# Performance work log

Hardware: AMD Instinct MI355X
Metric: run time of the kernel (lower is better)

Reference implementation:

```python
import jax, jax.numpy as jnp
import numpy as np

B, T, P, D, L = 16, 120, 96, 128, 2


def setup_inputs() -> dict:
    key = jax.random.key(0)
    k1, k2, k3, k4 = jax.random.split(key, 4)
    x = jax.random.normal(k1, (B, P, D, T), dtype=jnp.float32)
    # distances: symmetric-ish positive pairwise distances from random 3D points
    pts = jax.random.uniform(k2, (B, T, P, 3), dtype=jnp.float32) * 5.0
    diff = pts[:, :, :, None, :] - pts[:, :, None, :, :]
    distances = jnp.sqrt(jnp.sum(diff * diff, axis=-1) + 1e-12)
    # contiguous-prefix padding mask (matches the original self-loop loop semantics)
    counts = jax.random.randint(k3, (B,), P // 2, P + 1)
    padding_mask = jnp.arange(P)[None, :] < counts[:, None]
    # params: xavier_uniform with gain 1e-5 ~ tiny; bias 0; LN gamma=1, beta=0
    limit = 1e-5 * np.sqrt(6.0 / (D + D))
    W = jax.random.uniform(k4, (L, D, D), minval=-limit, maxval=limit, dtype=jnp.float32)
    b = jnp.zeros((L, D), dtype=jnp.float32)
    gamma = jnp.ones((L, D), dtype=jnp.float32)
    beta = jnp.zeros((L, D), dtype=jnp.float32)
    return {"x": x, "distances": distances, "padding_mask": padding_mask,
            "W": W, "b": b, "gamma": gamma, "beta": beta}


def _build_adjacency(distances, padding_mask):
    # valid_mask: [B,T,P,P]
    vm2d = (padding_mask[:, :, None] & padding_mask[:, None, :]).astype(distances.dtype)  # [B,P,P]
    vm = vm2d[:, None, :, :]
    vd = distances * vm
    pos = (vd > 0).astype(distances.dtype)
    n = jnp.sum(pos)
    mean = jnp.sum(vd * pos) / n
    var = jnp.sum(((vd - mean) ** 2) * pos) / (n - 1.0)  # unbiased, as torch.std
    sigma = jnp.sqrt(var) + 1e-8
    adj = jnp.exp(-(distances ** 2) / (2.0 * sigma ** 2)) * vm
    # self loops on valid (contiguous-prefix) nodes: add diag(mask)
    eye_mask = jnp.eye(P, dtype=distances.dtype)[None, :, :] * padding_mask[:, :, None].astype(distances.dtype)
    adj = adj + eye_mask[:, None, :, :]
    # symmetric normalization D^{-1/2} A D^{-1/2}
    deg = jnp.clip(jnp.sum(adj, axis=-1, keepdims=True), 1e-8, None)  # [B,T,P,1]
    deg = jnp.clip(deg * padding_mask[:, None, :, None].astype(distances.dtype), 1e-8, None)
    dis = deg ** -0.5
    adj = dis * adj * jnp.swapaxes(dis, -2, -1)
    return adj * vm


def _layer_norm_D(x, g, bt, eps=1e-5):
    # x: [B,P,D,T]; normalize over D axis
    mu = jnp.mean(x, axis=2, keepdims=True)
    var = jnp.mean((x - mu) ** 2, axis=2, keepdims=True)
    return (x - mu) * jax.lax.rsqrt(var + eps) * g[None, None, :, None] + bt[None, None, :, None]


def reference(x, distances, padding_mask, W, b, gamma, beta):
    adj = _build_adjacency(distances, padding_mask)  # [B,T,P,P]
    mask_f = padding_mask.astype(x.dtype)
    for l in range(L):
        xt = jnp.transpose(x, (0, 3, 1, 2))                      # [B,T,P,D]
        h = jnp.einsum('btpd,de->btpe', xt, W[l])                # x @ W
        o = jnp.einsum('btpq,btqd->btpd', adj, h)                # A @ xW
        o = jax.nn.relu(o + b[l])
        o = o * mask_f[:, None, :, None]
        o = jnp.transpose(o, (0, 2, 3, 1))                       # [B,P,D,T]
        o = _layer_norm_D(o, gamma[l], beta[l])
        x = x + o
    return x
```

## Files before the change

### kernel.cpp

```cpp
#include <hip/hip_runtime.h>
#include <math.h>

typedef __bf16 bf16_t;
typedef __bf16 bf16x8 __attribute__((ext_vector_type(8)));
typedef __bf16 bf16x4 __attribute__((ext_vector_type(4)));
typedef float f32x4 __attribute__((ext_vector_type(4)));

namespace {
constexpr int kB = 16;
constexpr int kT = 120;
constexpr int kP = 96;
constexpr int kD = 128;
constexpr int kBT = kB * kT;
constexpr int kPP = kP * kP;
constexpr int kPD = kP * kD;
constexpr long long kND = (long long)kBT * kPP;
constexpr unsigned kND4 = (unsigned)(kND / 4);

constexpr int TIN_TILES_PER_B = kPD / 32;
constexpr int TIN_BLOCKS = TIN_TILES_PER_B * kB;
constexpr int PREP_BLOCKS = 128;
constexpr int STATS_BLOCKS = 1024;
constexpr int FRONT_BLOCKS = TIN_BLOCKS + PREP_BLOCKS + STATS_BLOCKS;

constexpr int YS = 136;
constexpr int HS = 104;
constexpr int OS = 132;
constexpr int AS = 104;
constexpr int HT_OFF = 26112;
constexpr int AL_OFF = 52736;
constexpr int MROW_OFF = 72704;
constexpr int DIS_OFF = 73088;
constexpr int SMEM_B = 73472;
}

__device__ __forceinline__ f32x4 mfma16(bf16x8 a, bf16x8 b, f32x4 c) {
    return __builtin_amdgcn_mfma_f32_16x16x32_bf16(a, b, c, 0, 0, 0);
}

__global__ __launch_bounds__(256) void k_front(const float* __restrict__ x,
                                               bf16_t* __restrict__ y,
                                               const float* __restrict__ dist,
                                               const unsigned char* __restrict__ mraw,
                                               int* __restrict__ mask,
                                               double* __restrict__ stats,
                                               const float* __restrict__ W,
                                               bf16_t* __restrict__ wT) {
    __shared__ __align__(16) char sm[15488];
    const int bid = blockIdx.x;
    const int tid = threadIdx.x;

    if (bid < TIN_BLOCKS) {
        float* tile = (float*)sm;
        int b = bid / TIN_TILES_PER_B;
        int pd0 = (bid - b * TIN_TILES_PER_B) * 32;
        const float* xb = x + ((long long)b * kPD + pd0) * kT;
        #pragma unroll
        for (int k = 0; k < 4; ++k) {
            int idx = k * 256 + tid;
            if (idx < 960) {
                int r = idx / 30, c = idx - r * 30;
                float4 v = *(const float4*)(xb + idx * 4);
                tile[r * 121 + c * 4 + 0] = v.x;
                tile[r * 121 + c * 4 + 1] = v.y;
                tile[r * 121 + c * 4 + 2] = v.z;
                tile[r * 121 + c * 4 + 3] = v.w;
            }
        }
        __syncthreads();
        bf16_t* yb = y + (long long)b * kT * kPD + pd0;
        #pragma unroll
        for (int k = 0; k < 2; ++k) {
            int idx = k * 256 + tid;
            if (idx < 480) {
                int t = idx >> 2, dg = idx & 3;
                bf16x8 o;
                #pragma unroll
                for (int j = 0; j < 8; ++j) o[j] = (bf16_t)tile[(dg * 8 + j) * 121 + t];
                *(bf16x8*)(yb + (long long)t * kPD + dg * 8) = o;
            }
        }
    } else if (bid < TIN_BLOCKS + PREP_BLOCKS) {
        int pb = bid - TIN_BLOCKS;
        int l = pb >> 6;
        int idx = (pb & 63) * 256 + tid;
        int n = idx >> 7, k = idx & 127;
        wT[l * 16384 + n * 128 + k] = (bf16_t)W[l * 16384 + k * 128 + n];

        if (pb == 0) {
            const unsigned int* u32 = (const unsigned int*)mraw;
            unsigned int w0 = u32[0];
            int mode;
            if (w0 == 0x01010101u) mode = 0;
            else if (w0 == 1u) mode = 1;
            else mode = 2;
            for (int i = tid; i < kB * kP; i += 256) {
                int v;
                if (mode == 0)      v = (mraw[i] != 0);
                else if (mode == 1) v = (u32[i] != 0);
                else                v = (((const float*)mraw)[i] != 0.0f);
                mask[i] = v;
            }
        }
    } else {
        int sb = bid - TIN_BLOCKS - PREP_BLOCKS;
        int* ml = (int*)sm;
        double* sh = (double*)(sm + 6144);
        {
            const unsigned int* u32 = (const unsigned int*)mraw;
            unsigned int w0 = u32[0];
            int mode;
            if (w0 == 0x01010101u) mode = 0;
            else if (w0 == 1u) mode = 1;
            else mode = 2;
            for (int i = tid; i < kB * kP; i += 256) {
                int v;
                if (mode == 0)      v = (mraw[i] != 0);
                else if (mode == 1) v = (u32[i] != 0);
                else                v = (((const float*)mraw)[i] != 0.0f);
                ml[i] = v;
            }
        }
        __syncthreads();

        unsigned stride = (unsigned)STATS_BLOCKS * 256u;
        double s = 0.0, s2 = 0.0;
        int cnt = 0;
        for (unsigned i4 = (unsigned)sb * 256u + (unsigned)tid; i4 < kND4; i4 += stride) {
            unsigned q0 = (i4 % 24u) * 4u;
            unsigned r = i4 / 24u;
            unsigned p = r % 96u;
            unsigned b = r / (96u * 120u);
            const int* mb = ml + b * kP;
            if (mb[p]) {
                float4 d4 = *(const float4*)(dist + (size_t)i4 * 4);
                if (mb[q0 + 0]) { s += d4.x; s2 += (double)d4.x * d4.x; cnt++; }
                if (mb[q0 + 1]) { s += d4.y; s2 += (double)d4.y * d4.y; cnt++; }
                if (mb[q0 + 2]) { s += d4.z; s2 += (double)d4.z * d4.z; cnt++; }
                if (mb[q0 + 3]) { s += d4.w; s2 += (double)d4.w * d4.w; cnt++; }
            }
        }
        sh[tid] = s; __syncthreads();
        for (int off = 128; off > 0; off >>= 1) { if (tid < off) sh[tid] += sh[tid + off]; __syncthreads(); }
        if (tid == 0) atomicAdd(&stats[0], sh[0]);
        __syncthreads();
        sh[tid] = s2; __syncthreads();
        for (int off = 128; off > 0; off >>= 1) { if (tid < off) sh[tid] += sh[tid + off]; __syncthreads(); }
        if (tid == 0) atomicAdd(&stats[1], sh[0]);
        __syncthreads();
        sh[tid] = (double)cnt; __syncthreads();
        for (int off = 128; off > 0; off >>= 1) { if (tid < off) sh[tid] += sh[tid + off]; __syncthreads(); }
        if (tid == 0) atomicAdd(&stats[2], sh[0]);
    }
}

__global__ __launch_bounds__(256) void k_tout(const bf16_t* __restrict__ y,
                                              float* __restrict__ out) {
    __shared__ float tile[64 * 121];
    int b = blockIdx.y, pd0 = blockIdx.x * 64;
    int tid = threadIdx.x;
    const bf16_t* yb = y + (long long)b * kT * kPD + pd0;
    #pragma unroll
    for (int k = 0; k < 4; ++k) {
        int idx = k * 256 + tid;
        if (idx < 960) {
            int t = idx >> 3, dg = idx & 7;
            bf16x8 v = *(const bf16x8*)(yb + (long long)t * kPD + dg * 8);
            #pragma unroll
            for (int j = 0; j < 8; ++j) tile[(dg * 8 + j) * 121 + t] = (float)v[j];
        }
    }
    __syncthreads();
    float* ob = out + ((long long)b * kPD + pd0) * kT;
    #pragma unroll
    for (int k = 0; k < 8; ++k) {
        int idx = k * 256 + tid;
        if (idx < 1920) {
            int r = idx / 30, c = idx - r * 30;
            float4 v;
            v.x = tile[r * 121 + c * 4 + 0];
            v.y = tile[r * 121 + c * 4 + 1];
            v.z = tile[r * 121 + c * 4 + 2];
            v.w = tile[r * 121 + c * 4 + 3];
            *(float4*)(ob + r * kT + c * 4) = v;
        }
    }
}

__global__ __launch_bounds__(512, 2) void k_gcn(bf16_t* __restrict__ y,
                                                const float* __restrict__ dist,
                                                const int* __restrict__ mask,
                                                const double* __restrict__ stats,
                                                const bf16_t* __restrict__ wT,
                                                const float* __restrict__ bias,
                                                const float* __restrict__ gamma,
                                                const float* __restrict__ beta) {
    __shared__ __align__(16) char smem[SMEM_B];
    bf16_t* yL  = (bf16_t*)smem;
    bf16_t* hT  = (bf16_t*)(smem + HT_OFF);
    bf16_t* oLb = (bf16_t*)(smem + HT_OFF);
    float*  aT  = (float*)smem;
    bf16_t* aL  = (bf16_t*)(smem + AL_OFF);
    float* mrowf = (float*)(smem + MROW_OFF);
    float* dis   = (float*)(smem + DIS_OFF);

    const int tid = threadIdx.x;
    const int tx = tid & 15, ty = tid >> 4;
    const int lane = tid & 63, w = tid >> 6;
    const int wm = w >> 2, wn = w & 3;
    const int fc = lane & 15, fg = lane >> 4;
    const int bt = blockIdx.x, b = bt / kT;
    const int d0 = tx * 8;

    bf16_t* ybt = y + (size_t)bt * kPD;
    const float* dbt = dist + (size_t)bt * kPP;

    if (tid < kP) mrowf[tid] = (float)mask[b * kP + tid];

    double sn = stats[2];
    double mean = stats[0] / sn;
    double var = (stats[1] - sn * mean * mean) / (sn - 1.0);
    double sg = sqrt(var) + 1e-8;
    float inv2s2 = (float)(1.0 / (2.0 * sg * sg));

    __syncthreads();

    #pragma unroll
    for (int k = 0; k < 5; ++k) {
        int i4 = k * 512 + tid;
        if (i4 < 2304) {
            int e = i4 * 4;
            int p = e / kP, q = e - p * kP;
            float4 d4 = *(const float4*)(dbt + e);
            float mp = mrowf[p];
            float vv[4];
            vv[0] = (mp * mrowf[q + 0] != 0.f) ? __expf(-d4.x * d4.x * inv2s2) : 0.f;
            vv[1] = (mp * mrowf[q + 1] != 0.f) ? __expf(-d4.y * d4.y * inv2s2) : 0.f;
            vv[2] = (mp * mrowf[q + 2] != 0.f) ? __expf(-d4.z * d4.z * inv2s2) : 0.f;
            vv[3] = (mp * mrowf[q + 3] != 0.f) ? __expf(-d4.w * d4.w * inv2s2) : 0.f;
            #pragma unroll
            for (int j = 0; j < 4; ++j) {
                if (p == q + j) vv[j] += mp;
                aT[p * 100 + q + j] = vv[j];
            }
        }
    }
    __syncthreads();

    if (tid < kP) {
        float s = 0.f;
        for (int q = 0; q < kP; ++q) s += aT[q * 100 + tid];
        s = fmaxf(s, 1e-8f);
        s = fmaxf(s * mrowf[tid], 1e-8f);
        dis[tid] = rsqrtf(s);
    }
    __syncthreads();

    #pragma unroll
    for (int k = 0; k < 5; ++k) {
        int i4 = k * 512 + tid;
        if (i4 < 2304) {
            int e = i4 * 4;
            int p = e / kP, q = e - p * kP;
            float dp = dis[p];
            bf16x4 ov;
            #pragma unroll
            for (int j = 0; j < 4; ++j)
                ov[j] = (bf16_t)(dp * aT[p * 100 + q + j] * dis[q + j]);
            *(bf16x4*)(aL + p * AS + q) = ov;
        }
    }
    __syncthreads();

    #pragma unroll
    for (int i = 0; i < 3; ++i) {
        int p = ty * 3 + i;
        *(bf16x8*)(yL + p * YS + d0) = *(const bf16x8*)(ybt + p * kD + d0);
    }

    for (int l = 0; l < 2; ++l) {
        const bf16_t* wTl = wT + l * kD * kD;
        bf16x8 wf[4][2];
        #pragma unroll
        for (int kt = 0; kt < 4; ++kt) {
            wf[kt][0] = *(const bf16x8*)(wTl + ((wn * 2 + 0) * 16 + fc) * kD + kt * 32 + fg * 8);
            wf[kt][1] = *(const bf16x8*)(wTl + ((wn * 2 + 1) * 16 + fc) * kD + kt * 32 + fg * 8);
        }
        __syncthreads();

        f32x4 acc[3][2];
        #pragma unroll
        for (int mt = 0; mt < 3; ++mt) { acc[mt][0] = {0,0,0,0}; acc[mt][1] = {0,0,0,0}; }
        #pragma unroll
        for (int kt = 0; kt < 4; ++kt) {
            #pragma unroll
            for (int mt = 0; mt < 3; ++mt) {
                bf16x8 af = *(const bf16x8*)(yL + ((wm * 3 + mt) * 16 + fc) * YS + kt * 32 + fg * 8);
                acc[mt][0] = mfma16(af, wf[kt][0], acc[mt][0]);
                acc[mt][1] = mfma16(af, wf[kt][1], acc[mt][1]);
            }
        }
        #pragma unroll
        for (int mt = 0; mt < 3; ++mt)
            #pragma unroll
            for (int nn = 0; nn < 2; ++nn) {
                int e = (wn * 2 + nn) * 16 + fc;
                int p0 = (wm * 3 + mt) * 16 + fg * 4;
                bf16x4 hv = {(bf16_t)acc[mt][nn][0], (bf16_t)acc[mt][nn][1],
                             (bf16_t)acc[mt][nn][2], (bf16_t)acc[mt][nn][3]};
                *(bf16x4*)(hT + e * HS + p0) = hv;
            }
        __syncthreads();

        f32x4 acc2[3][2];
        #pragma unroll
        for (int mt = 0; mt < 3; ++mt) { acc2[mt][0] = {0,0,0,0}; acc2[mt][1] = {0,0,0,0}; }
        #pragma unroll
        for (int kt = 0; kt < 3; ++kt) {
            bf16x8 bf0 = *(const bf16x8*)(hT + ((wn * 2 + 0) * 16 + fc) * HS + kt * 32 + fg * 8);
            bf16x8 bf1 = *(const bf16x8*)(hT + ((wn * 2 + 1) * 16 + fc) * HS + kt * 32 + fg * 8);
            #pragma unroll
            for (int mt = 0; mt < 3; ++mt) {
                bf16x8 af = *(const bf16x8*)(aL + ((wm * 3 + mt) * 16 + fc) * AS + kt * 32 + fg * 8);
                acc2[mt][0] = mfma16(af, bf0, acc2[mt][0]);
                acc2[mt][1] = mfma16(af, bf1, acc2[mt][1]);
            }
        }
        __syncthreads();

        #pragma unroll
        for (int mt = 0; mt < 3; ++mt)
            #pragma unroll
            for (int nn = 0; nn < 2; ++nn) {
                int d = (wn * 2 + nn) * 16 + fc;
                int p0 = (wm * 3 + mt) * 16 + fg * 4;
                oLb[(p0 + 0) * OS + d] = (bf16_t)acc2[mt][nn][0];
                oLb[(p0 + 1) * OS + d] = (bf16_t)acc2[mt][nn][1];
                oLb[(p0 + 2) * OS + d] = (bf16_t)acc2[mt][nn][2];
                oLb[(p0 + 3) * OS + d] = (bf16_t)acc2[mt][nn][3];
            }
        __syncthreads();

        const float* bl = bias + l * kD;
        const float* gl = gamma + l * kD;
        const float* bel = beta + l * kD;
        float4 bb0 = *(const float4*)(bl + d0), bb1 = *(const float4*)(bl + d0 + 4);
        float4 gg0 = *(const float4*)(gl + d0), gg1 = *(const float4*)(gl + d0 + 4);
        float4 be0 = *(const float4*)(bel + d0), be1 = *(const float4*)(bel + d0 + 4);
        float bb[8] = {bb0.x, bb0.y, bb0.z, bb0.w, bb1.x, bb1.y, bb1.z, bb1.w};
        float gg[8] = {gg0.x, gg0.y, gg0.z, gg0.w, gg1.x, gg1.y, gg1.z, gg1.w};
        float be[8] = {be0.x, be0.y, be0.z, be0.w, be1.x, be1.y, be1.z, be1.w};

        #pragma unroll
        for (int i = 0; i < 3; ++i) {
            int p = ty * 3 + i;
            float mpf = mrowf[p];
            bf16x4 o0 = *(const bf16x4*)(oLb + p * OS + d0);
            bf16x4 o1 = *(const bf16x4*)(oLb + p * OS + d0 + 4);
            bf16x8 yv = *(const bf16x8*)(yL + p * YS + d0);
            float v[8];
            #pragma unroll
            for (int j = 0; j < 4; ++j) {
                v[j]     = fmaxf((float)o0[j] + bb[j], 0.f) * mpf;
                v[j + 4] = fmaxf((float)o1[j] + bb[j + 4], 0.f) * mpf;
            }
            float s = v[0] + v[1] + v[2] + v[3] + v[4] + v[5] + v[6] + v[7];
            s += __shfl_xor(s, 8);
            s += __shfl_xor(s, 4);
            s += __shfl_xor(s, 2);
            s += __shfl_xor(s, 1);
            float mu = s * 0.0078125f;

            float ss = 0.f;
            #pragma unroll
            for (int j = 0; j < 8; ++j) { float dv = v[j] - mu; ss += dv * dv; }
            ss += __shfl_xor(ss, 8);
            ss += __shfl_xor(ss, 4);
            ss += __shfl_xor(ss, 2);
            ss += __shfl_xor(ss, 1);
            float inv = rsqrtf(ss * 0.0078125f + 1e-5f);

            bf16x8 c;
            #pragma unroll
            for (int j = 0; j < 8; ++j)
                c[j] = (bf16_t)((float)yv[j] + (v[j] - mu) * inv * gg[j] + be[j]);

            if (l == 0) {
                *(bf16x8*)(yL + p * YS + d0) = c;
            } else {
                *(bf16x8*)(ybt + p * kD + d0) = c;
            }
        }
    }
}

extern "C" void kernel_launch(void* const* d_in, const int* in_sizes, int n_in,
                              void* d_out, int out_size, void* d_ws, size_t ws_size,
                              hipStream_t stream) {
    (void)in_sizes; (void)n_in; (void)out_size; (void)ws_size;

    const float* x = (const float*)d_in[0];
    const float* dist = (const float*)d_in[1];
    const unsigned char* mraw = (const unsigned char*)d_in[2];
    const float* W = (const float*)d_in[3];
    const float* bias = (const float*)d_in[4];
    const float* gamma = (const float*)d_in[5];
    const float* beta = (const float*)d_in[6];
    float* out = (float*)d_out;

    char* ws = (char*)d_ws;
    double* stats = (double*)ws;
    int* mask = (int*)(ws + 64);
    bf16_t* wT = (bf16_t*)(ws + 8192);
    bf16_t* y = (bf16_t*)(ws + 81920);

    hipMemsetAsync(stats, 0, 32, stream);

    k_front<<<FRONT_BLOCKS, 256, 0, stream>>>(x, y, dist, mraw, mask, stats, W, wT);

    k_gcn<<<kBT, 512, 0, stream>>>(y, dist, mask, stats, wT, bias, gamma, beta);

    k_tout<<<dim3(kPD / 64, kB), 256, 0, stream>>>(y, out);
}
```

Before: 177.0 us.

## Prefetch transpose tiles across multiple 64-row tiles per block and double stats blocks

The x-transpose part of the front kernel now handles 64-row tiles, three per block, and holds the next tile's global loads in registers while the current tile is written out. This is meant to overlap global loads with the LDS transpose and to cut block count and launch overhead. The prep blocks now come first in the grid order, and the stats section gets twice as many blocks, presumably for more parallelism in the reduction. The trade-offs are higher register and shared memory use per block (30976 bytes of LDS), which may lower occupancy, and a reliance on the stats code handling the new block count correctly.

```diff
diff --git a/kernel.cpp b/kernel.cpp
--- a/kernel.cpp
+++ b/kernel.cpp
@@ -17,11 +17,12 @@
 constexpr long long kND = (long long)kBT * kPP;
 constexpr unsigned kND4 = (unsigned)(kND / 4);
 
-constexpr int TIN_TILES_PER_B = kPD / 32;
-constexpr int TIN_BLOCKS = TIN_TILES_PER_B * kB;
 constexpr int PREP_BLOCKS = 128;
-constexpr int STATS_BLOCKS = 1024;
-constexpr int FRONT_BLOCKS = TIN_BLOCKS + PREP_BLOCKS + STATS_BLOCKS;
+constexpr int TIN_TILES = (kPD / 64) * kB;
+constexpr int TILES_PER_BLOCK = 3;
+constexpr int TIN_BLOCKS = TIN_TILES / TILES_PER_BLOCK;
+constexpr int STATS_BLOCKS = 2048;
+constexpr int FRONT_BLOCKS = PREP_BLOCKS + TIN_BLOCKS + STATS_BLOCKS;
 
 constexpr int YS = 136;
 constexpr int HS = 104;
@@ -46,42 +47,12 @@
                                                double* __restrict__ stats,
                                                const float* __restrict__ W,
                                                bf16_t* __restrict__ wT) {
-    __shared__ __align__(16) char sm[15488];
+    __shared__ __align__(16) char sm[30976];
     const int bid = blockIdx.x;
     const int tid = threadIdx.x;
 
-    if (bid < TIN_BLOCKS) {
-        float* tile = (float*)sm;
-        int b = bid / TIN_TILES_PER_B;
-        int pd0 = (bid - b * TIN_TILES_PER_B) * 32;
-        const float* xb = x + ((long long)b * kPD + pd0) * kT;
-        #pragma unroll
-        for (int k = 0; k < 4; ++k) {
-            int idx = k * 256 + tid;
-            if (idx < 960) {
-                int r = idx / 30, c = idx - r * 30;
-                float4 v = *(const float4*)(xb + idx * 4);
-                tile[r * 121 + c * 4 + 0] = v.x;
-                tile[r * 121 + c * 4 + 1] = v.y;
-                tile[r * 121 + c * 4 + 2] = v.z;
-                tile[r * 121 + c * 4 + 3] = v.w;
-            }
-        }
-        __syncthreads();
-        bf16_t* yb = y + (long long)b * kT * kPD + pd0;
-        #pragma unroll
-        for (int k = 0; k < 2; ++k) {
-            int idx = k * 256 + tid;
-            if (idx < 480) {
-                int t = idx >> 2, dg = idx & 3;
-                bf16x8 o;
-                #pragma unroll
-                for (int j = 0; j < 8; ++j) o[j] = (bf16_t)tile[(dg * 8 + j) * 121 + t];
-                *(bf16x8*)(yb + (long long)t * kPD + dg * 8) = o;
-            }
-        }
-    } else if (bid < TIN_BLOCKS + PREP_BLOCKS) {
-        int pb = bid - TIN_BLOCKS;
+    if (bid < PREP_BLOCKS) {
+        int pb = bid;
         int l = pb >> 6;
         int idx = (pb & 63) * 256 + tid;
         int n = idx >> 7, k = idx & 127;
@@ -102,8 +73,61 @@
                 mask[i] = v;
             }
         }
+    } else if (bid < PREP_BLOCKS + TIN_BLOCKS) {
+        float* tile = (float*)sm;
+        int tb = bid - PREP_BLOCKS;
+        int tile0 = tb * TILES_PER_BLOCK;
+
+        float4 pf[8];
+        {
+            const float* xb = x + (long long)tile0 * 7680;
+            #pragma unroll
+            for (int k = 0; k < 8; ++k) {
+                int idx = k * 256 + tid;
+                if (idx < 1920) pf[k] = *(const float4*)(xb + idx * 4);
+            }
+        }
+
+        for (int it = 0; it < TILES_PER_BLOCK; ++it) {
+            int tg = tile0 + it;
+            #pragma unroll
+            for (int k = 0; k < 8; ++k) {
+                int idx = k * 256 + tid;
+                if (idx < 1920) {
+                    int r = idx / 30, c = (idx - r * 30) * 4;
+                    tile[r * 121 + c + 0] = pf[k].x;
+                    tile[r * 121 + c + 1] = pf[k].y;
+                    tile[r * 121 + c + 2] = pf[k].z;
+                    tile[r * 121 + c + 3] = pf[k].w;
+                }
+            }
+            __syncthreads();
+            if (it + 1 < TILES_PER_BLOCK) {
+                const float* xb = x + (long long)(tg + 1) * 7680;
+                #pragma unroll
+                for (int k = 0; k < 8; ++k) {
+                    int idx = k * 256 + tid;
+                    if (idx < 1920) pf[k] = *(const float4*)(xb + idx * 4);
+                }
+            }
+            int b = tg / (kPD / 64);
+            int pd0 = (tg - b * (kPD / 64)) * 64;
+            bf16_t* yb = y + (long long)b * kT * kPD + pd0;
+            #pragma unroll
+            for (int k = 0; k < 4; ++k) {
+                int idx = k * 256 + tid;
+                if (idx < 960) {
+                    int t = idx >> 3, dg = idx & 7;
+                    bf16x8 o;
+                    #pragma unroll
+                    for (int j = 0; j < 8; ++j) o[j] = (bf16_t)tile[(dg * 8 + j) * 121 + t];
+                    *(bf16x8*)(yb + (long long)t * kPD + dg * 8) = o;
+                }
+            }
+            __syncthreads();
+        }
     } else {
-        int sb = bid - TIN_BLOCKS - PREP_BLOCKS;
+        int sb = bid - PREP_BLOCKS - TIN_BLOCKS;
         int* ml = (int*)sm;
         double* sh = (double*)(sm + 6144);
         {
```

Measured after the change: 207.4 us. 1.17x slower.
